# Performance work log

Measured on AMD Instinct MI355X. Metric: run time of the kernel, lower is better.

The kernel has to match this reference:

```python
import jax, jax.numpy as jnp
import numpy as np

C, H, N, B, L = 1, 512, 64, 16, 2048  # n_channels, n_heads, d_kernel, batch, seq_len


def setup_inputs() -> dict:
    key = jax.random.key(0)
    k1, k2 = jax.random.split(key)
    u = jax.random.normal(k1, (B, C * H, L), dtype=jnp.float32)
    k = jax.random.normal(k2, (C, H, N), dtype=jnp.float32)
    return {"u": u, "k": k}


def _l1_normalize(x, axis):
    # torch.linalg.norm(x, ord=1, dim=axis, keepdim=True): vector 1-norm along `axis`
    return x / jnp.sum(jnp.abs(x), axis=axis, keepdims=True)


def _forward(u, k):
    c, h, n = k.shape
    bsz, d, l = u.shape  # d == c*h
    dt = u.dtype
    # Shift matrix A: A[:, :, 1:, :-1] = I  (companion-style shift)
    A = jnp.zeros((c, h, n, n), dtype=dt).at[:, :, 1:, :-1].set(jnp.eye(n - 1, dtype=dt))
    # b = e1 broadcast to (c, h, n)
    b_vec = jnp.zeros((c, h, n), dtype=dt).at[:, :, 0].set(1.0)
    # closed-loop: k_norm = L1-normalize(clamp(k, 1/16, 1)); A_cl = L1-normalize(A + b k^T)
    k_norm = _l1_normalize(jnp.clip(k, 1.0 / 16.0, 1.0), axis=2)
    BK = jnp.einsum('chi,chj->chij', b_vec, k_norm)
    M = _l1_normalize(A + BK, axis=2)

    # Krylov recurrence: f[i] = k . (M^i b), i = 0..l-1
    def step(x, _):
        f_i = jnp.einsum('chn,chn->ch', k, x)
        x_next = jnp.einsum('chij,chj->chi', M, x)
        return x_next, f_i

    _, f = jax.lax.scan(step, b_vec, None, length=l)  # f: (l, c, h)
    f = jnp.moveaxis(f, 0, -1)  # (c, h, l)

    # Causal FFT convolution of u (b, c, h, l) with filter f (c, h, l)
    n_fft = 2 * l
    uf = jnp.fft.rfft(u.reshape(bsz, c, h, l), n=n_fft)
    ff = jnp.fft.rfft(f, n=n_fft)
    y = jnp.fft.irfft(uf * ff[None], n=n_fft)[..., :l]
    return y.reshape(bsz, c * h, l)


def reference(u, k):
    return _forward(u, k)
```

## Files before the change

kernel.cpp:

```cpp
#include <hip/hip_runtime.h>


namespace {

constexpr int kH = 512;
constexpr int kL = 2048;
constexpr int kChunks = 32;

typedef __attribute__((ext_vector_type(8))) short bf16x8;
typedef __attribute__((ext_vector_type(4))) float f32x4;

#define MFMA(A, B, C) __builtin_amdgcn_mfma_f32_16x16x32_bf16((A), (B), (C), 0, 0, 0)

__device__ inline unsigned int cvt_pk_bf16(float lo, float hi) {
  unsigned int r;
  asm("v_cvt_pk_bf16_f32 %0, %1, %2" : "=v"(r) : "v"(lo), "v"(hi));
  return r;
}

union B8U4 { bf16x8 v; unsigned int u[4]; };

__device__ inline void cvt_split8(const f32x4 a, const f32x4 b, bf16x8& fh, bf16x8& fl) {
  B8U4 H, L;
  float x[8];
  #pragma unroll
  for (int j = 0; j < 4; ++j) { x[j] = a[j]; x[4 + j] = b[j]; }
  #pragma unroll
  for (int d = 0; d < 4; ++d) {
    const float x0 = x[2 * d], x1 = x[2 * d + 1];
    const unsigned int hp = cvt_pk_bf16(x0, x1);
    const float h0 = __uint_as_float(hp << 16);
    const float h1 = __uint_as_float(hp & 0xFFFF0000u);
    H.u[d] = hp;
    L.u[d] = cvt_pk_bf16(x0 - h0, x1 - h1);
  }
  fh = H.v; fl = L.v;
}

__device__ inline void gen_frag(const float* tp, int n0, bf16x8& fh, bf16x8& fl) {
  float t[8];
  #pragma unroll
  for (int j = 0; j < 8; ++j) {
    const int n = n0 - j;
    t[j] = (n >= 0 && n < 127) ? tp[n] : 0.0f;
  }
  const f32x4 a = {t[0], t[1], t[2], t[3]};
  const f32x4 b = {t[4], t[5], t[6], t[7]};
  cvt_split8(a, b, fh, fl);
}

__device__ inline void gen_fragB(const float* tp, int base, bf16x8& fh, bf16x8& fl) {
  float t[8];
  #pragma unroll
  for (int j = 0; j < 8; ++j) t[j] = tp[base + j];
  const f32x4 a = {t[0], t[1], t[2], t[3]};
  const f32x4 b = {t[4], t[5], t[6], t[7]};
  cvt_split8(a, b, fh, fl);
}


__global__ __launch_bounds__(256, 1)
void ssm_mfma_kernel(const float* __restrict__ u,
                     const float* __restrict__ kin,
                     float* __restrict__ y) {
  const int h    = blockIdx.x;
  const int tid  = threadIdx.x;
  const int wid  = tid >> 6;
  const int lane = tid & 63;
  const int ln16 = lane & 15;
  const int quad = lane >> 4;

  __shared__ alignas(16) char pool[36864];
  auto Astage  = (float (*)[68]) (pool);
  auto Pstage  = (float (*)[68]) (pool + 17408);
  auto sring   = (float (*)[16][68]) (pool);
  auto cring   = (float (*)[16][68]) (pool + 13056);
  auto yuring  = (float (*)[16][68]) (pool + 21760);
  auto taps    = (float (*)[128]) (pool + 34816);
  float* wPad  = (float*) (pool + 36352);

  if (wid == 0) {
    const float kv = kin[h * 64 + lane];
    const float kc = fminf(fmaxf(kv, 0.0625f), 1.0f);
    float ks = kc;
    #pragma unroll
    for (int off = 32; off >= 1; off >>= 1) ks += __shfl_xor(ks, off);
    const float kn = kc / ks;
    const float cc = 1.0f / (1.0f + kn);
    float pp = cc;
    #pragma unroll
    for (int off = 1; off < 64; off <<= 1) {
      const float t = __shfl_up(pp, off);
      if (lane >= off) pp *= t;
    }
    float Pe = __shfl_up(pp, 1);
    if (lane == 0) Pe = 1.0f;
    const float wv = (lane < 63) ? (kn * cc * Pe) : Pe;
    const float gv = kv * Pe;
    float sv = (lane == 0) ? 1.0f : 0.0f;
    for (int rr = 0; rr < 63; ++rr) {
      const float s0 = __shfl(sv, rr);
      const float cf = __shfl(wv, lane - 1 - rr);
      if (lane > rr) sv = fmaf(cf, s0, sv);
    }
    taps[0][lane] = 0.0f;
    taps[1][lane] = 0.0f;
    const float gn = __shfl(gv, lane + 1);
    taps[2][lane] = (lane < 63) ? gn : 0.0f;
    taps[2][64 + lane] = 0.0f;
    taps[0][63 + lane] = sv;
    taps[1][63 + lane] = gv;
    if (lane == 0) { taps[0][127] = 0.0f; taps[1][127] = 0.0f; }
    wPad[lane] = wv;
    wPad[64 + lane] = 0.0f;
  }
  __syncthreads();

  {
    const int mt = wid;
    bf16x8 xh[2], xl[2], g2h[2], g2l[2];
    #pragma unroll
    for (int tk = 0; tk < 2; ++tk) {
      const int n0 = 16 * mt + ln16 - (32 * tk + 8 * quad) + 63;
      gen_frag(taps[0], n0, xh[tk], xl[tk]);
      gen_frag(taps[1], n0, g2h[tk], g2l[tk]);
    }
    #pragma unroll
    for (int nt = 0; nt < 4; ++nt) {
      f32x4 accA = {0.f, 0.f, 0.f, 0.f};
      f32x4 accG = {0.f, 0.f, 0.f, 0.f};
      #pragma unroll
      for (int tk = 0; tk < 2; ++tk) {
        const int base = 8 * quad + 32 * tk - (16 * nt + ln16) + 63;
        bf16x8 bh, bl;
        gen_fragB(wPad, base, bh, bl);
        accA = MFMA(xh[tk], bh, accA);
        accA = MFMA(xh[tk], bl, accA);
        accA = MFMA(xl[tk], bh, accA);
        accA = MFMA(xl[tk], bl, accA);
        bf16x8 sbh, sbl;
        gen_fragB(taps[0], base, sbh, sbl);
        accG = MFMA(g2h[tk], sbh, accG);
        accG = MFMA(g2h[tk], sbl, accG);
        accG = MFMA(g2l[tk], sbh, accG);
      }
      #pragma unroll
      for (int r = 0; r < 4; ++r) {
        Astage[16 * mt + 4 * quad + r][16 * nt + ln16] = accA[r];
        Pstage[16 * mt + 4 * quad + r][16 * nt + ln16] = accG[r];
      }
    }
  }
  __syncthreads();

  bf16x8 oxH[4][2], oxL[4][2];
  if (wid == 2) {
    #pragma unroll
    for (int mt = 0; mt < 4; ++mt) {
      #pragma unroll
      for (int tk = 0; tk < 2; ++tk) {
        const int n0 = 16 * mt + ln16 - (32 * tk + 8 * quad) + 63;
        gen_frag(taps[0], n0, oxH[mt][tk], oxL[mt][tk]);
      }
    }
  } else if (wid == 3) {
    #pragma unroll
    for (int mt = 0; mt < 4; ++mt) {
      #pragma unroll
      for (int tk = 0; tk < 2; ++tk) {
        const int row = 16 * mt + ln16, k0 = 32 * tk + 8 * quad;
        const f32x4 a = *(const f32x4*)&Pstage[row][k0];
        const f32x4 b = *(const f32x4*)&Pstage[row][k0 + 4];
        cvt_split8(a, b, oxH[mt][tk], oxL[mt][tk]);
      }
    }
  }
  __syncthreads();

  {
    const int mt = wid;
    bf16x8 g2h[2], g2l[2];
    #pragma unroll
    for (int tk = 0; tk < 2; ++tk) {
      const int n0 = 16 * mt + ln16 - (32 * tk + 8 * quad) + 63;
      gen_frag(taps[1], n0, g2h[tk], g2l[tk]);
    }
    #pragma unroll
    for (int nt = 0; nt < 4; ++nt) {
      f32x4 acc = {0.f, 0.f, 0.f, 0.f};
      #pragma unroll
      for (int tk = 0; tk < 2; ++tk) {
        float t[8];
        #pragma unroll
        for (int j = 0; j < 8; ++j)
          t[j] = Astage[8 * quad + 32 * tk + j][16 * nt + ln16];
        const f32x4 a = {t[0], t[1], t[2], t[3]};
        const f32x4 b = {t[4], t[5], t[6], t[7]};
        bf16x8 bh, bl;
        cvt_split8(a, b, bh, bl);
        acc = MFMA(g2h[tk], bh, acc);
        acc = MFMA(g2h[tk], bl, acc);
        acc = MFMA(g2l[tk], bh, acc);
      }
      #pragma unroll
      for (int r = 0; r < 4; ++r) {
        const int i = 16 * mt + 4 * quad + r, j = 16 * nt + ln16;
        Pstage[i][j] = acc[r] + taps[2][(i - j) + 63];
      }
    }
  }
  __syncthreads();

  if (wid == 0) {
    #pragma unroll
    for (int mt = 0; mt < 4; ++mt) {
      #pragma unroll
      for (int tk = 0; tk < 2; ++tk) {
        const int row = 16 * mt + ln16, k0 = 32 * tk + 8 * quad;
        const f32x4 a = *(const f32x4*)&Astage[row][k0];
        const f32x4 b = *(const f32x4*)&Astage[row][k0 + 4];
        cvt_split8(a, b, oxH[mt][tk], oxL[mt][tk]);
      }
    }
  } else if (wid == 1) {
    #pragma unroll
    for (int mt = 0; mt < 4; ++mt) {
      #pragma unroll
      for (int tk = 0; tk < 2; ++tk) {
        const int row = 16 * mt + ln16, k0 = 32 * tk + 8 * quad;
        const f32x4 a = *(const f32x4*)&Pstage[row][k0];
        const f32x4 b = *(const f32x4*)&Pstage[row][k0 + 4];
        cvt_split8(a, b, oxH[mt][tk], oxL[mt][tk]);
      }
    }
  }
  __syncthreads();

  bf16x8 opH[2], opL[2];
  {
    bf16x8 z;
    #pragma unroll
    for (int j = 0; j < 8; ++j) z[j] = 0;
    opH[0] = z; opH[1] = z; opL[0] = z; opL[1] = z;
  }

  const float* ub = u + ((size_t)ln16 * kH + h) * kL + 8 * quad;
  float* yb = y + ((size_t)ln16 * kH + h) * kL;

  f32x4 uv[4];
  if (wid >= 2) {
    #pragma unroll
    for (int i = 0; i < 4; ++i)
      uv[i] = *(const f32x4*)(ub + 32 * (i >> 1) + 4 * (i & 1));
  }

  #pragma unroll 1
  for (int s = 0; s < kChunks + 2; ++s) {
    const int m3  = s % 3;
    const int m3a = (m3 == 2) ? 0 : m3 + 1;
    const int m3b = (m3 == 0) ? 2 : m3 - 1;
    if (wid >= 2) {
      if (s < kChunks) {
        cvt_split8(uv[0], uv[1], opH[0], opL[0]);
        cvt_split8(uv[2], uv[3], opH[1], opL[1]);
        const int tn = (s + 1 < kChunks) ? 64 * (s + 1) : 0;
        #pragma unroll
        for (int i = 0; i < 4; ++i)
          uv[i] = *(const f32x4*)(ub + tn + 32 * (i >> 1) + 4 * (i & 1));
        f32x4 acc[4] = {};
        #pragma unroll
        for (int mt = 0; mt < 4; ++mt) {
          #pragma unroll
          for (int tk = 0; tk < 2; ++tk) {
            acc[mt] = MFMA(oxH[mt][tk], opH[tk], acc[mt]);
            acc[mt] = MFMA(oxH[mt][tk], opL[tk], acc[mt]);
            acc[mt] = MFMA(oxL[mt][tk], opH[tk], acc[mt]);
          }
        }
        float* dst = (wid == 2) ? &cring[s & 1][0][0] : &yuring[m3][0][0];
        #pragma unroll
        for (int mt = 0; mt < 4; ++mt)
          *(f32x4*)&dst[ln16 * 68 + 16 * mt + 4 * quad] = acc[mt];
      }
    } else if (wid == 0) {
      if (s >= 1 && s <= kChunks) {
        if (s >= 2) {
          #pragma unroll
          for (int tk = 0; tk < 2; ++tk) {
            const int k0 = 8 * quad + 32 * tk;
            const f32x4 ra = *(const f32x4*)&sring[m3a][ln16][k0];
            const f32x4 rb = *(const f32x4*)&sring[m3a][ln16][k0 + 4];
            cvt_split8(ra, rb, opH[tk], opL[tk]);
          }
        }
        f32x4 acc[4];
        #pragma unroll
        for (int mt = 0; mt < 4; ++mt)
          acc[mt] = *(const f32x4*)&cring[(s - 1) & 1][ln16][16 * mt + 4 * quad];
        #pragma unroll
        for (int mt = 0; mt < 4; ++mt) {
          #pragma unroll
          for (int tk = 0; tk < 2; ++tk) {
            acc[mt] = MFMA(oxH[mt][tk], opH[tk], acc[mt]);
            acc[mt] = MFMA(oxH[mt][tk], opL[tk], acc[mt]);
            acc[mt] = MFMA(oxL[mt][tk], opH[tk], acc[mt]);
          }
        }
        #pragma unroll
        for (int mt = 0; mt < 4; ++mt)
          *(f32x4*)&sring[m3b][ln16][16 * mt + 4 * quad] = acc[mt];
      }
    } else {
      if (s >= 2) {
        if (s >= 3) {
          #pragma unroll
          for (int tk = 0; tk < 2; ++tk) {
            const int k0 = 8 * quad + 32 * tk;
            const f32x4 ra = *(const f32x4*)&sring[m3][ln16][k0];
            const f32x4 rb = *(const f32x4*)&sring[m3][ln16][k0 + 4];
            cvt_split8(ra, rb, opH[tk], opL[tk]);
          }
        }
        f32x4 acc[4];
        #pragma unroll
        for (int mt = 0; mt < 4; ++mt)
          acc[mt] = *(const f32x4*)&yuring[m3a][ln16][16 * mt + 4 * quad];
        #pragma unroll
        for (int mt = 0; mt < 4; ++mt) {
          #pragma unroll
          for (int tk = 0; tk < 2; ++tk) {
            acc[mt] = MFMA(oxH[mt][tk], opH[tk], acc[mt]);
            acc[mt] = MFMA(oxH[mt][tk], opL[tk], acc[mt]);
            acc[mt] = MFMA(oxL[mt][tk], opH[tk], acc[mt]);
          }
        }
        #pragma unroll
        for (int mt = 0; mt < 4; ++mt)
          *(f32x4*)(yb + 64 * (s - 2) + 16 * mt + 4 * quad) = acc[mt];
      }
    }
    asm volatile("s_waitcnt lgkmcnt(0)" ::: "memory");
    __builtin_amdgcn_s_barrier();
    asm volatile("" ::: "memory");
  }
}

}

extern "C" void kernel_launch(void* const* d_in, const int* in_sizes, int n_in,
                              void* d_out, int out_size, void* d_ws, size_t ws_size,
                              hipStream_t stream) {
  const float* u  = (const float*)d_in[0];
  const float* kk = (const float*)d_in[1];
  if (n_in >= 2 && in_sizes[0] < in_sizes[1]) {
    const float* t = u; u = kk; kk = t;
  }
  float* yy = (float*)d_out;
  hipLaunchKernelGGL(ssm_mfma_kernel, dim3(kH), dim3(256), 0, stream, u, kk, yy);
}
```

Measured before the change: 145.9 us.

## Split sequence across waves with chunked state scan instead of wave-specialized pipeline

Replaces the three-stage per-wave pipeline over 32 chunks with a chunk-parallel scheme. Each of the four waves processes 8 consecutive chunks. A first local pass computes each wave's end state, then a short cross-wave prefix combines these states using powers of the transition matrix (A^8, computed by repeated squaring). A second pass recomputes the states and emits outputs. The serial dependency chain per block shrinks and barriers drop out of the main loop, at the cost of roughly doubling the MFMA work and using more LDS. Launch bounds now request two blocks per CU.

```diff
diff --git a/kernel.cpp b/kernel.cpp
--- a/kernel.cpp
+++ b/kernel.cpp
@@ -5,7 +5,6 @@
 
 constexpr int kH = 512;
 constexpr int kL = 2048;
-constexpr int kChunks = 32;
 
 typedef __attribute__((ext_vector_type(8))) short bf16x8;
 typedef __attribute__((ext_vector_type(4))) float f32x4;
@@ -58,8 +57,7 @@
   cvt_split8(a, b, fh, fl);
 }
 
-
-__global__ __launch_bounds__(256, 1)
+__global__ __launch_bounds__(256, 2)
 void ssm_mfma_kernel(const float* __restrict__ u,
                      const float* __restrict__ kin,
                      float* __restrict__ y) {
@@ -70,14 +68,23 @@
   const int ln16 = lane & 15;
   const int quad = lane >> 4;
 
-  __shared__ alignas(16) char pool[36864];
-  auto Astage  = (float (*)[68]) (pool);
-  auto Pstage  = (float (*)[68]) (pool + 17408);
-  auto sring   = (float (*)[16][68]) (pool);
-  auto cring   = (float (*)[16][68]) (pool + 13056);
-  auto yuring  = (float (*)[16][68]) (pool + 21760);
-  auto taps    = (float (*)[128]) (pool + 34816);
-  float* wPad  = (float*) (pool + 36352);
+  __shared__ alignas(16) char pool[69632];
+  auto taps = (float (*)[128]) (pool);
+  float* wPad = (float*) (pool + 1536);
+  auto stA = (float (*)[68]) (pool + 2048);
+  auto stB = (float (*)[68]) (pool + 19456);
+  auto scr = (float (*)[68]) (pool + 2048 + wid * 4352);
+  auto sT  = (bf16x8 (*)[2][2][64]) (pool + 36864);
+  auto g1T = (bf16x8 (*)[2][2][64]) (pool + 53248);
+  auto g2T = (bf16x8 (*)[2][2][64]) (pool + 19456);
+
+  const int cb = 8 * wid;
+  const float* ub = u + ((size_t)ln16 * kH + h) * kL + 8 * quad;
+  float* yb = y + ((size_t)ln16 * kH + h) * kL;
+  f32x4 uv[4];
+  #pragma unroll
+  for (int i = 0; i < 4; ++i)
+    uv[i] = *(const f32x4*)(ub + 64 * cb + 32 * (i >> 1) + 4 * (i & 1));
 
   if (wid == 0) {
     const float kv = kin[h * 64 + lane];
@@ -117,231 +124,357 @@
   __syncthreads();
 
   {
-    const int mt = wid;
-    bf16x8 xh[2], xl[2], g2h[2], g2l[2];
-    #pragma unroll
-    for (int tk = 0; tk < 2; ++tk) {
-      const int n0 = 16 * mt + ln16 - (32 * tk + 8 * quad) + 63;
-      gen_frag(taps[0], n0, xh[tk], xl[tk]);
-      gen_frag(taps[1], n0, g2h[tk], g2l[tk]);
-    }
-    #pragma unroll
-    for (int nt = 0; nt < 4; ++nt) {
-      f32x4 accA = {0.f, 0.f, 0.f, 0.f};
-      f32x4 accG = {0.f, 0.f, 0.f, 0.f};
-      #pragma unroll
-      for (int tk = 0; tk < 2; ++tk) {
-        const int base = 8 * quad + 32 * tk - (16 * nt + ln16) + 63;
+    bf16x8 sH[4][2], sL[4][2];
+    #pragma unroll
+    for (int mt = 0; mt < 4; ++mt) {
+      #pragma unroll
+      for (int tk = 0; tk < 2; ++tk) {
+        const int n0 = 16 * mt + ln16 - (32 * tk + 8 * quad) + 63;
+        gen_frag(taps[0], n0, sH[mt][tk], sL[mt][tk]);
+      }
+    }
+    #pragma unroll
+    for (int mt = 0; mt < 4; ++mt) {
+      f32x4 acc = {0.f, 0.f, 0.f, 0.f};
+      #pragma unroll
+      for (int tk = 0; tk < 2; ++tk) {
+        const int base = 8 * quad + 32 * tk - (16 * wid + ln16) + 63;
         bf16x8 bh, bl;
         gen_fragB(wPad, base, bh, bl);
-        accA = MFMA(xh[tk], bh, accA);
-        accA = MFMA(xh[tk], bl, accA);
-        accA = MFMA(xl[tk], bh, accA);
-        accA = MFMA(xl[tk], bl, accA);
-        bf16x8 sbh, sbl;
-        gen_fragB(taps[0], base, sbh, sbl);
-        accG = MFMA(g2h[tk], sbh, accG);
-        accG = MFMA(g2h[tk], sbl, accG);
-        accG = MFMA(g2l[tk], sbh, accG);
-      }
-      #pragma unroll
-      for (int r = 0; r < 4; ++r) {
-        Astage[16 * mt + 4 * quad + r][16 * nt + ln16] = accA[r];
-        Pstage[16 * mt + 4 * quad + r][16 * nt + ln16] = accG[r];
-      }
+        acc = MFMA(sH[mt][tk], bh, acc);
+        acc = MFMA(sH[mt][tk], bl, acc);
+        acc = MFMA(sL[mt][tk], bh, acc);
+        acc = MFMA(sL[mt][tk], bl, acc);
+      }
+      #pragma unroll
+      for (int r = 0; r < 4; ++r)
+        stA[16 * mt + 4 * quad + r][16 * wid + ln16] = acc[r];
+    }
+    #pragma unroll
+    for (int tk = 0; tk < 2; ++tk) {
+      const int n0 = 16 * wid + ln16 - (32 * tk + 8 * quad) + 63;
+      bf16x8 fh, fl;
+      gen_frag(taps[0], n0, fh, fl);
+      sT[wid][tk][0][lane] = fh;  sT[wid][tk][1][lane] = fl;
+      gen_frag(taps[2], n0, fh, fl);
+      g1T[wid][tk][0][lane] = fh; g1T[wid][tk][1][lane] = fl;
     }
   }
   __syncthreads();
 
-  bf16x8 oxH[4][2], oxL[4][2];
-  if (wid == 2) {
-    #pragma unroll
-    for (int mt = 0; mt < 4; ++mt) {
-      #pragma unroll
-      for (int tk = 0; tk < 2; ++tk) {
-        const int n0 = 16 * mt + ln16 - (32 * tk + 8 * quad) + 63;
-        gen_frag(taps[0], n0, oxH[mt][tk], oxL[mt][tk]);
-      }
-    }
-  } else if (wid == 3) {
-    #pragma unroll
-    for (int mt = 0; mt < 4; ++mt) {
+  bf16x8 aH[4][2], aL[4][2];
+  #pragma unroll
+  for (int mt = 0; mt < 4; ++mt) {
+    #pragma unroll
+    for (int tk = 0; tk < 2; ++tk) {
+      const int row = 16 * mt + ln16, k0 = 32 * tk + 8 * quad;
+      cvt_split8(*(const f32x4*)&stA[row][k0], *(const f32x4*)&stA[row][k0 + 4],
+                 aH[mt][tk], aL[mt][tk]);
+    }
+  }
+  #pragma unroll
+  for (int mt = 0; mt < 4; ++mt) {
+    f32x4 acc = {0.f, 0.f, 0.f, 0.f};
+    #pragma unroll
+    for (int tk = 0; tk < 2; ++tk) {
+      float t[8];
+      #pragma unroll
+      for (int j = 0; j < 8; ++j)
+        t[j] = stA[8 * quad + 32 * tk + j][16 * wid + ln16];
+      const f32x4 a = {t[0], t[1], t[2], t[3]};
+      const f32x4 b = {t[4], t[5], t[6], t[7]};
+      bf16x8 bh, bl;
+      cvt_split8(a, b, bh, bl);
+      acc = MFMA(aH[mt][tk], bh, acc);
+      acc = MFMA(aH[mt][tk], bl, acc);
+      acc = MFMA(aL[mt][tk], bh, acc);
+      acc = MFMA(aL[mt][tk], bl, acc);
+    }
+    #pragma unroll
+    for (int r = 0; r < 4; ++r)
+      stB[16 * mt + 4 * quad + r][16 * wid + ln16] = acc[r];
+  }
+  __syncthreads();
+
+  #pragma unroll
+  for (int sq = 0; sq < 2; ++sq) {
+    float (*src)[68] = (sq == 0) ? stB : stA;
+    float (*dst)[68] = (sq == 0) ? stA : stB;
+    #pragma unroll
+    for (int mt = 0; mt < 4; ++mt) {
+      bf16x8 rh[2], rl[2];
       #pragma unroll
       for (int tk = 0; tk < 2; ++tk) {
         const int row = 16 * mt + ln16, k0 = 32 * tk + 8 * quad;
-        const f32x4 a = *(const f32x4*)&Pstage[row][k0];
-        const f32x4 b = *(const f32x4*)&Pstage[row][k0 + 4];
-        cvt_split8(a, b, oxH[mt][tk], oxL[mt][tk]);
-      }
-    }
-  }
-  __syncthreads();
-
-  {
-    const int mt = wid;
-    bf16x8 g2h[2], g2l[2];
-    #pragma unroll
-    for (int tk = 0; tk < 2; ++tk) {
-      const int n0 = 16 * mt + ln16 - (32 * tk + 8 * quad) + 63;
-      gen_frag(taps[1], n0, g2h[tk], g2l[tk]);
-    }
-    #pragma unroll
-    for (int nt = 0; nt < 4; ++nt) {
+        cvt_split8(*(const f32x4*)&src[row][k0], *(const f32x4*)&src[row][k0 + 4],
+                   rh[tk], rl[tk]);
+      }
       f32x4 acc = {0.f, 0.f, 0.f, 0.f};
       #pragma unroll
       for (int tk = 0; tk < 2; ++tk) {
         float t[8];
         #pragma unroll
         for (int j = 0; j < 8; ++j)
-          t[j] = Astage[8 * quad + 32 * tk + j][16 * nt + ln16];
+          t[j] = src[8 * quad + 32 * tk + j][16 * wid + ln16];
         const f32x4 a = {t[0], t[1], t[2], t[3]};
         const f32x4 b = {t[4], t[5], t[6], t[7]};
         bf16x8 bh, bl;
         cvt_split8(a, b, bh, bl);
-        acc = MFMA(g2h[tk], bh, acc);
-        acc = MFMA(g2h[tk], bl, acc);
-        acc = MFMA(g2l[tk], bh, acc);
-      }
-      #pragma unroll
-      for (int r = 0; r < 4; ++r) {
-        const int i = 16 * mt + 4 * quad + r, j = 16 * nt + ln16;
-        Pstage[i][j] = acc[r] + taps[2][(i - j) + 63];
-      }
-    }
-  }
-  __syncthreads();
-
-  if (wid == 0) {
-    #pragma unroll
-    for (int mt = 0; mt < 4; ++mt) {
-      #pragma unroll
-      for (int tk = 0; tk < 2; ++tk) {
-        const int row = 16 * mt + ln16, k0 = 32 * tk + 8 * quad;
-        const f32x4 a = *(const f32x4*)&Astage[row][k0];
-        const f32x4 b = *(const f32x4*)&Astage[row][k0 + 4];
-        cvt_split8(a, b, oxH[mt][tk], oxL[mt][tk]);
-      }
-    }
-  } else if (wid == 1) {
-    #pragma unroll
-    for (int mt = 0; mt < 4; ++mt) {
-      #pragma unroll
-      for (int tk = 0; tk < 2; ++tk) {
-        const int row = 16 * mt + ln16, k0 = 32 * tk + 8 * quad;
-        const f32x4 a = *(const f32x4*)&Pstage[row][k0];
-        const f32x4 b = *(const f32x4*)&Pstage[row][k0 + 4];
-        cvt_split8(a, b, oxH[mt][tk], oxL[mt][tk]);
-      }
-    }
-  }
-  __syncthreads();
-
-  bf16x8 opH[2], opL[2];
+        acc = MFMA(rh[tk], bh, acc);
+        acc = MFMA(rh[tk], bl, acc);
+        acc = MFMA(rl[tk], bh, acc);
+        acc = MFMA(rl[tk], bl, acc);
+      }
+      #pragma unroll
+      for (int r = 0; r < 4; ++r)
+        dst[16 * mt + 4 * quad + r][16 * wid + ln16] = acc[r];
+    }
+    __syncthreads();
+  }
+
+  bf16x8 pH[2], pL[2];
   {
     bf16x8 z;
     #pragma unroll
     for (int j = 0; j < 8; ++j) z[j] = 0;
-    opH[0] = z; opH[1] = z; opL[0] = z; opL[1] = z;
-  }
-
-  const float* ub = u + ((size_t)ln16 * kH + h) * kL + 8 * quad;
-  float* yb = y + ((size_t)ln16 * kH + h) * kL;
-
-  f32x4 uv[4];
-  if (wid >= 2) {
-    #pragma unroll
-    for (int i = 0; i < 4; ++i)
-      uv[i] = *(const f32x4*)(ub + 32 * (i >> 1) + 4 * (i & 1));
+    pH[0] = z; pH[1] = z; pL[0] = z; pL[1] = z;
   }
 
   #pragma unroll 1
-  for (int s = 0; s < kChunks + 2; ++s) {
-    const int m3  = s % 3;
-    const int m3a = (m3 == 2) ? 0 : m3 + 1;
-    const int m3b = (m3 == 0) ? 2 : m3 - 1;
-    if (wid >= 2) {
-      if (s < kChunks) {
-        cvt_split8(uv[0], uv[1], opH[0], opL[0]);
-        cvt_split8(uv[2], uv[3], opH[1], opL[1]);
-        const int tn = (s + 1 < kChunks) ? 64 * (s + 1) : 0;
+  for (int i = 0; i < 8; ++i) {
+    bf16x8 uH[2], uL[2];
+    cvt_split8(uv[0], uv[1], uH[0], uL[0]);
+    cvt_split8(uv[2], uv[3], uH[1], uL[1]);
+    const int tn = 64 * ((i < 7) ? (cb + i + 1) : cb);
+    #pragma unroll
+    for (int q = 0; q < 4; ++q)
+      uv[q] = *(const f32x4*)(ub + tn + 32 * (q >> 1) + 4 * (q & 1));
+
+    f32x4 acc[4];
+    #pragma unroll
+    for (int mt = 0; mt < 4; ++mt) acc[mt] = (f32x4){0.f, 0.f, 0.f, 0.f};
+    #pragma unroll
+    for (int mt = 0; mt < 4; ++mt) {
+      #pragma unroll
+      for (int tk = 0; tk < 2; ++tk) {
+        acc[mt] = MFMA(aH[mt][tk], pH[tk], acc[mt]);
+        acc[mt] = MFMA(aH[mt][tk], pL[tk], acc[mt]);
+        acc[mt] = MFMA(aL[mt][tk], pH[tk], acc[mt]);
+      }
+      #pragma unroll
+      for (int tk = 0; tk < 2; ++tk) {
+        const bf16x8 th = sT[mt][tk][0][lane];
+        const bf16x8 tl = sT[mt][tk][1][lane];
+        acc[mt] = MFMA(th, uH[tk], acc[mt]);
+        acc[mt] = MFMA(th, uL[tk], acc[mt]);
+        acc[mt] = MFMA(tl, uH[tk], acc[mt]);
+      }
+    }
+    #pragma unroll
+    for (int mt = 0; mt < 4; ++mt)
+      *(f32x4*)&scr[ln16][16 * mt + 4 * quad] = acc[mt];
+    asm volatile("s_waitcnt lgkmcnt(0)" ::: "memory");
+    __builtin_amdgcn_sched_barrier(0);
+    #pragma unroll
+    for (int tk = 0; tk < 2; ++tk) {
+      const int k0 = 8 * quad + 32 * tk;
+      cvt_split8(*(const f32x4*)&scr[ln16][k0], *(const f32x4*)&scr[ln16][k0 + 4],
+                 pH[tk], pL[tk]);
+    }
+  }
+
+  asm volatile("s_waitcnt lgkmcnt(0)" ::: "memory");
+  __builtin_amdgcn_s_barrier();
+  asm volatile("" ::: "memory");
+
+  bf16x8 c0H[2], c0L[2];
+  f32x4 sac1[4], sac2[4];
+  {
+    float (*s0)[68] = (float (*)[68])(pool + 2048);
+    float (*s1)[68] = (float (*)[68])(pool + 2048 + 4352);
+    float (*s2)[68] = (float (*)[68])(pool + 2048 + 2 * 4352);
+    if (wid == 1) {
+      #pragma unroll
+      for (int tk = 0; tk < 2; ++tk) {
+        const int k0 = 8 * quad + 32 * tk;
+        cvt_split8(*(const f32x4*)&s0[ln16][k0], *(const f32x4*)&s0[ln16][k0 + 4],
+                   pH[tk], pL[tk]);
+      }
+    } else if (wid == 2) {
+      #pragma unroll
+      for (int tk = 0; tk < 2; ++tk) {
+        const int k0 = 8 * quad + 32 * tk;
+        cvt_split8(*(const f32x4*)&s0[ln16][k0], *(const f32x4*)&s0[ln16][k0 + 4],
+                   c0H[tk], c0L[tk]);
+      }
+      #pragma unroll
+      for (int mt = 0; mt < 4; ++mt)
+        sac1[mt] = *(const f32x4*)&s1[ln16][16 * mt + 4 * quad];
+    } else if (wid == 3) {
+      #pragma unroll
+      for (int tk = 0; tk < 2; ++tk) {
+        const int k0 = 8 * quad + 32 * tk;
+        cvt_split8(*(const f32x4*)&s0[ln16][k0], *(const f32x4*)&s0[ln16][k0 + 4],
+                   c0H[tk], c0L[tk]);
+      }
+      #pragma unroll
+      for (int mt = 0; mt < 4; ++mt) {
+        sac1[mt] = *(const f32x4*)&s1[ln16][16 * mt + 4 * quad];
+        sac2[mt] = *(const f32x4*)&s2[ln16][16 * mt + 4 * quad];
+      }
+    }
+  }
+  asm volatile("s_waitcnt lgkmcnt(0)" ::: "memory");
+  __builtin_amdgcn_s_barrier();
+  asm volatile("" ::: "memory");
+
+  if (wid == 0) {
+    bf16x8 z;
+    #pragma unroll
+    for (int j = 0; j < 8; ++j) z[j] = 0;
+    pH[0] = z; pH[1] = z; pL[0] = z; pL[1] = z;
+  } else if (wid >= 2) {
+    #pragma unroll
+    for (int mt = 0; mt < 4; ++mt) {
+      bf16x8 a8h[2], a8l[2];
+      #pragma unroll
+      for (int tk = 0; tk < 2; ++tk) {
+        const int row = 16 * mt + ln16, k0 = 32 * tk + 8 * quad;
+        cvt_split8(*(const f32x4*)&stB[row][k0], *(const f32x4*)&stB[row][k0 + 4],
+                   a8h[tk], a8l[tk]);
+      }
+      #pragma unroll
+      for (int tk = 0; tk < 2; ++tk) {
+        sac1[mt] = MFMA(a8h[tk], c0H[tk], sac1[mt]);
+        sac1[mt] = MFMA(a8h[tk], c0L[tk], sac1[mt]);
+        sac1[mt] = MFMA(a8l[tk], c0H[tk], sac1[mt]);
+        sac1[mt] = MFMA(a8l[tk], c0L[tk], sac1[mt]);
+      }
+    }
+    #pragma unroll
+    for (int mt = 0; mt < 4; ++mt)
+      *(f32x4*)&scr[ln16][16 * mt + 4 * quad] = sac1[mt];
+    asm volatile("s_waitcnt lgkmcnt(0)" ::: "memory");
+    __builtin_amdgcn_sched_barrier(0);
+    #pragma unroll
+    for (int tk = 0; tk < 2; ++tk) {
+      const int k0 = 8 * quad + 32 * tk;
+      cvt_split8(*(const f32x4*)&scr[ln16][k0], *(const f32x4*)&scr[ln16][k0 + 4],
+                 pH[tk], pL[tk]);
+    }
+    if (wid == 3) {
+      #pragma unroll
+      for (int mt = 0; mt < 4; ++mt) {
+        bf16x8 a8h[2], a8l[2];
         #pragma unroll
-        for (int i = 0; i < 4; ++i)
-          uv[i] = *(const f32x4*)(ub + tn + 32 * (i >> 1) + 4 * (i & 1));
-        f32x4 acc[4] = {};
-        #pragma unroll
-        for (int mt = 0; mt < 4; ++mt) {
-          #pragma unroll
-          for (int tk = 0; tk < 2; ++tk) {
-            acc[mt] = MFMA(oxH[mt][tk], opH[tk], acc[mt]);
-            acc[mt] = MFMA(oxH[mt][tk], opL[tk], acc[mt]);
-            acc[mt] = MFMA(oxL[mt][tk], opH[tk], acc[mt]);
-          }
-        }
-        float* dst = (wid == 2) ? &cring[s & 1][0][0] : &yuring[m3][0][0];
-        #pragma unroll
-        for (int mt = 0; mt < 4; ++mt)
-          *(f32x4*)&dst[ln16 * 68 + 16 * mt + 4 * quad] = acc[mt];
-      }
-    } else if (wid == 0) {
-      if (s >= 1 && s <= kChunks) {
-        if (s >= 2) {
-          #pragma unroll
-          for (int tk = 0; tk < 2; ++tk) {
-            const int k0 = 8 * quad + 32 * tk;
-            const f32x4 ra = *(const f32x4*)&sring[m3a][ln16][k0];
-            const f32x4 rb = *(const f32x4*)&sring[m3a][ln16][k0 + 4];
-            cvt_split8(ra, rb, opH[tk], opL[tk]);
-          }
-        }
-        f32x4 acc[4];
-        #pragma unroll
-        for (int mt = 0; mt < 4; ++mt)
-          acc[mt] = *(const f32x4*)&cring[(s - 1) & 1][ln16][16 * mt + 4 * quad];
-        #pragma unroll
-        for (int mt = 0; mt < 4; ++mt) {
-          #pragma unroll
-          for (int tk = 0; tk < 2; ++tk) {
-            acc[mt] = MFMA(oxH[mt][tk], opH[tk], acc[mt]);
-            acc[mt] = MFMA(oxH[mt][tk], opL[tk], acc[mt]);
-            acc[mt] = MFMA(oxL[mt][tk], opH[tk], acc[mt]);
-          }
+        for (int tk = 0; tk < 2; ++tk) {
+          const int row = 16 * mt + ln16, k0 = 32 * tk + 8 * quad;
+          cvt_split8(*(const f32x4*)&stB[row][k0], *(const f32x4*)&stB[row][k0 + 4],
+                     a8h[tk], a8l[tk]);
         }
         #pragma unroll
-        for (int mt = 0; mt < 4; ++mt)
-          *(f32x4*)&sring[m3b][ln16][16 * mt + 4 * quad] = acc[mt];
-      }
-    } else {
-      if (s >= 2) {
-        if (s >= 3) {
-          #pragma unroll
-          for (int tk = 0; tk < 2; ++tk) {
-            const int k0 = 8 * quad + 32 * tk;
-            const f32x4 ra = *(const f32x4*)&sring[m3][ln16][k0];
-            const f32x4 rb = *(const f32x4*)&sring[m3][ln16][k0 + 4];
-            cvt_split8(ra, rb, opH[tk], opL[tk]);
-          }
+        for (int tk = 0; tk < 2; ++tk) {
+          sac2[mt] = MFMA(a8h[tk], pH[tk], sac2[mt]);
+          sac2[mt] = MFMA(a8h[tk], pL[tk], sac2[mt]);
+          sac2[mt] = MFMA(a8l[tk], pH[tk], sac2[mt]);
+          sac2[mt] = MFMA(a8l[tk], pL[tk], sac2[mt]);
         }
-        f32x4 acc[4];
-        #pragma unroll
-        for (int mt = 0; mt < 4; ++mt)
-          acc[mt] = *(const f32x4*)&yuring[m3a][ln16][16 * mt + 4 * quad];
-        #pragma unroll
-        for (int mt = 0; mt < 4; ++mt) {
-          #pragma unroll
-          for (int tk = 0; tk < 2; ++tk) {
-            acc[mt] = MFMA(oxH[mt][tk], opH[tk], acc[mt]);
-            acc[mt] = MFMA(oxH[mt][tk], opL[tk], acc[mt]);
-            acc[mt] = MFMA(oxL[mt][tk], opH[tk], acc[mt]);
-          }
-        }
-        #pragma unroll
-        for (int mt = 0; mt < 4; ++mt)
-          *(f32x4*)(yb + 64 * (s - 2) + 16 * mt + 4 * quad) = acc[mt];
+      }
+      #pragma unroll
+      for (int mt = 0; mt < 4; ++mt)
+        *(f32x4*)&scr[ln16][16 * mt + 4 * quad] = sac2[mt];
+      asm volatile("s_waitcnt lgkmcnt(0)" ::: "memory");
+      __builtin_amdgcn_sched_barrier(0);
+      #pragma unroll
+      for (int tk = 0; tk < 2; ++tk) {
+        const int k0 = 8 * quad + 32 * tk;
+        cvt_split8(*(const f32x4*)&scr[ln16][k0], *(const f32x4*)&scr[ln16][k0 + 4],
+                   pH[tk], pL[tk]);
+      }
+    }
+  }
+  asm volatile("s_waitcnt lgkmcnt(0)" ::: "memory");
+  __builtin_amdgcn_s_barrier();
+  asm volatile("" ::: "memory");
+
+  #pragma unroll
+  for (int tk = 0; tk < 2; ++tk) {
+    const int n0 = 16 * wid + ln16 - (32 * tk + 8 * quad) + 63;
+    bf16x8 fh, fl;
+    gen_frag(taps[1], n0, fh, fl);
+    g2T[wid][tk][0][lane] = fh;  g2T[wid][tk][1][lane] = fl;
+  }
+  asm volatile("s_waitcnt lgkmcnt(0)" ::: "memory");
+  __builtin_amdgcn_s_barrier();
+  asm volatile("" ::: "memory");
+
+  #pragma unroll 1
+  for (int i = 0; i < 8; ++i) {
+    bf16x8 uH[2], uL[2];
+    cvt_split8(uv[0], uv[1], uH[0], uL[0]);
+    cvt_split8(uv[2], uv[3], uH[1], uL[1]);
+    const int tn = 64 * ((i < 7) ? (cb + i + 1) : cb);
+    #pragma unroll
+    for (int q = 0; q < 4; ++q)
+      uv[q] = *(const f32x4*)(ub + tn + 32 * (q >> 1) + 4 * (q & 1));
+
+    f32x4 accR[4], accY[4];
+    #pragma unroll
+    for (int mt = 0; mt < 4; ++mt) {
+      accR[mt] = (f32x4){0.f, 0.f, 0.f, 0.f};
+      accY[mt] = (f32x4){0.f, 0.f, 0.f, 0.f};
+    }
+    #pragma unroll
+    for (int mt = 0; mt < 4; ++mt) {
+      #pragma unroll
+      for (int tk = 0; tk < 2; ++tk) {
+        accR[mt] = MFMA(aH[mt][tk], pH[tk], accR[mt]);
+        accR[mt] = MFMA(aH[mt][tk], pL[tk], accR[mt]);
+        accR[mt] = MFMA(aL[mt][tk], pH[tk], accR[mt]);
+      }
+      #pragma unroll
+      for (int tk = 0; tk < 2; ++tk) {
+        const bf16x8 th = sT[mt][tk][0][lane];
+        const bf16x8 tl = sT[mt][tk][1][lane];
+        accR[mt] = MFMA(th, uH[tk], accR[mt]);
+        accR[mt] = MFMA(th, uL[tk], accR[mt]);
+        accR[mt] = MFMA(tl, uH[tk], accR[mt]);
+      }
+    }
+    #pragma unroll
+    for (int mt = 0; mt < 4; ++mt)
+      *(f32x4*)&scr[ln16][16 * mt + 4 * quad] = accR[mt];
+    #pragma unroll
+    for (int mt = 0; mt < 4; ++mt) {
+      #pragma unroll
+      for (int tk = 0; tk < 2; ++tk) {
+        const bf16x8 gh = g1T[mt][tk][0][lane];
+        const bf16x8 gl = g1T[mt][tk][1][lane];
+        accY[mt] = MFMA(gh, pH[tk], accY[mt]);
+        accY[mt] = MFMA(gh, pL[tk], accY[mt]);
+        accY[mt] = MFMA(gl, pH[tk], accY[mt]);
       }
     }
     asm volatile("s_waitcnt lgkmcnt(0)" ::: "memory");
-    __builtin_amdgcn_s_barrier();
-    asm volatile("" ::: "memory");
+    __builtin_amdgcn_sched_barrier(0);
+    #pragma unroll
+    for (int tk = 0; tk < 2; ++tk) {
+      const int k0 = 8 * quad + 32 * tk;
+      cvt_split8(*(const f32x4*)&scr[ln16][k0], *(const f32x4*)&scr[ln16][k0 + 4],
+                 pH[tk], pL[tk]);
+    }
+    #pragma unroll
+    for (int mt = 0; mt < 4; ++mt) {
+      #pragma unroll
+      for (int tk = 0; tk < 2; ++tk) {
+        const bf16x8 gh = g2T[mt][tk][0][lane];
+        const bf16x8 gl = g2T[mt][tk][1][lane];
+        accY[mt] = MFMA(gh, pH[tk], accY[mt]);
+        accY[mt] = MFMA(gh, pL[tk], accY[mt]);
+        accY[mt] = MFMA(gl, pH[tk], accY[mt]);
+      }
+      *(f32x4*)(yb + 64 * (cb + i) + 16 * mt + 4 * quad) = accY[mt];
+    }
   }
 }
 
```

Result: no change. 148.0 us (+1.5%).
